# Kernel optimization log

Measured on AMD Instinct MI355X. Metric: run time of the kernel, lower is better.

The kernel has to match this reference:

```python
import jax, jax.numpy as jnp
import numpy as np
import math

B, S, HID, NH = 2, 2048, 1024, 16
HD = HID // NH


def setup_inputs() -> dict:
    key = jax.random.key(0)
    ks = jax.random.split(key, 6)
    scale = 0.02
    return {
        "hidden_states": jax.random.normal(ks[0], (B, S, HID), dtype=jnp.float32),
        "attention_mask": jnp.ones((B, S), dtype=jnp.float32),
        "Wq": jax.random.normal(ks[1], (HID, HID), dtype=jnp.float32) * scale,
        "bq": jnp.zeros((HID,), dtype=jnp.float32),
        "Wk": jax.random.normal(ks[2], (HID, HID), dtype=jnp.float32) * scale,
        "bk": jnp.zeros((HID,), dtype=jnp.float32),
        "Wv": jax.random.normal(ks[3], (HID, HID), dtype=jnp.float32) * scale,
        "bv": jnp.zeros((HID,), dtype=jnp.float32),
        "Wo": jax.random.normal(ks[4], (HID, HID), dtype=jnp.float32) * scale,
        "bo": jnp.zeros((HID,), dtype=jnp.float32),
        "beta": jnp.zeros((1,), dtype=jnp.float32),
        "gamma": jnp.ones((1,), dtype=jnp.float32),
    }


def reference(hidden_states, attention_mask, Wq, bq, Wk, bk, Wv, bv, Wo, bo, beta, gamma):
    b, s, h = hidden_states.shape

    def proj(W, bias):
        # torch Linear: x @ W.T + b ; then split heads -> [B, NH, S, HD]
        y = jnp.einsum('bsh,oh->bso', hidden_states, W) + bias
        return y.reshape(b, s, NH, HD).transpose(0, 2, 1, 3)

    q = proj(Wq, bq)
    k = proj(Wk, bk)
    v = proj(Wv, bv)

    scores = jnp.einsum('bnsd,bntd->bnst', q, k) / math.sqrt(HD)  # [B,NH,S,S]
    # extended mask: [B,1,1,S]; additive -1e4 on masked positions
    scores = scores + (1.0 - attention_mask)[:, None, None, :] * (-10000.0)

    # ConsMax: exp(scores - beta - rowmax) / gamma (no sum normalization)
    shifted = scores - beta
    shifted = shifted - jnp.max(shifted, axis=-1, keepdims=True)
    probs = jnp.exp(shifted) / gamma  # dropout p=0 -> identity

    ctx = jnp.einsum('bnst,bntd->bnsd', probs, v)  # [B,NH,S,HD]
    ctx = ctx.transpose(0, 2, 1, 3).reshape(b, s, h)
    return jnp.einsum('bsh,oh->bso', ctx, Wo) + bo
```

## Files before the change

kernel.cpp:

```cpp
#include <hip/hip_runtime.h>
#include <hip/hip_bf16.h>


typedef unsigned short u16;
typedef __attribute__((ext_vector_type(8))) short short8;
typedef __attribute__((ext_vector_type(4))) float floatx4;
typedef __attribute__((ext_vector_type(16))) float floatx16;

constexpr int B_  = 2;
constexpr int S_  = 2048;
constexpr int HID = 1024;
constexpr int NH  = 16;
constexpr int HD  = 64;

constexpr float LOG2E   = 1.4426950408889634f;
constexpr float QSCALE  = 0.125f * LOG2E;
constexpr float MSCALE  = -10000.0f * LOG2E;

#if __has_builtin(__builtin_amdgcn_exp2f)
#define EXP2(x) __builtin_amdgcn_exp2f(x)
#else
#define EXP2(x) exp2f(x)
#endif

__device__ __forceinline__ u16 f2us(float f) {
    union { float f; unsigned int i; } x;
    x.f = f;
    unsigned int r = x.i + 0x7FFFu + ((x.i >> 16) & 1u);
    return (u16)(r >> 16);
}
__device__ __forceinline__ unsigned pk2(float a, float b) {
    __hip_bfloat162 h = __float22bfloat162_rn(make_float2(a, b));
    unsigned u; __builtin_memcpy(&u, &h, 4); return u;
}
__device__ __forceinline__ void async_lds16(const u16* g, u16* l) {
    __builtin_amdgcn_global_load_lds(
        (const __attribute__((address_space(1))) unsigned int*)g,
        (__attribute__((address_space(3))) unsigned int*)l, 16, 0, 0);
}

__global__ __launch_bounds__(256)
void cvt_all(const float* __restrict__ hs, const float* __restrict__ Wq,
             const float* __restrict__ Wk, const float* __restrict__ Wv,
             const float* __restrict__ Wo,
             u16* __restrict__ hs_bf, u16* __restrict__ Wcat,
             u16* __restrict__ Wo_bf)
{
    const int bid = blockIdx.x;
    const float* src;
    u16* dst;
    size_t base;
    if (bid < 4096) {
        src = hs; dst = hs_bf; base = (size_t)bid * 1024;
    } else if (bid < 7168) {
        const int s = (bid - 4096) >> 10;
        src = (s == 0) ? Wq : (s == 1) ? Wk : Wv;
        dst = Wcat + (size_t)s * 1048576;
        base = (size_t)((bid - 4096) & 1023) * 1024;
    } else {
        src = Wo; dst = Wo_bf; base = (size_t)(bid - 7168) * 1024;
    }
    const size_t i = base + threadIdx.x * 4;
    float4 t = *(const float4*)(src + i);
    uint2 o = { pk2(t.x, t.y), pk2(t.z, t.w) };
    *(uint2*)(dst + i) = o;
}

__global__ __launch_bounds__(256)
void qkv_gemm(const u16* __restrict__ hs_bf, const u16* __restrict__ Wcat,
              const float* __restrict__ bq, const float* __restrict__ bk,
              const float* __restrict__ bv,
              u16* __restrict__ Qo, u16* __restrict__ Ko, u16* __restrict__ VT)
{
    __shared__ u16 Alds[8192];
    __shared__ u16 Blds[8192];

    const int tid = threadIdx.x;
    const int id  = blockIdx.x;
    const int xcd = id & 7, jb = id >> 3;
    const int m0  = (xcd * 4 + (jb & 3)) * 128;
    const int n0g = (jb >> 2) * 128;
    const int p   = n0g >> 10;
    const int n0  = n0g & 1023;
    const u16*   Wb = Wcat + (size_t)p * 1048576;
    const float* bi = (p == 0) ? bq : (p == 1) ? bk : bv;
    const float  osc = (p == 0) ? QSCALE : 1.0f;

    const int w = tid >> 6, l = tid & 63;
    const int quad = l >> 4, l16 = l & 15;
    const int wy = w >> 1, wx = w & 1;

    floatx4 acc[4][4];
    #pragma unroll
    for (int i = 0; i < 4; ++i)
        #pragma unroll
        for (int j = 0; j < 4; ++j) acc[i][j] = (floatx4){0.f, 0.f, 0.f, 0.f};

    for (int k0 = 0; k0 < HID; k0 += 64) {
        __syncthreads();
        #pragma unroll
        for (int c = 0; c < 2; ++c) {
            const int s = w * 2 + c;
            #pragma unroll
            for (int t = 0; t < 2; ++t) {
                async_lds16(hs_bf + (size_t)(m0 + s * 16 + l16) * HID + k0 + t * 32 + quad * 8,
                            &Alds[s * 1024 + t * 512]);
                async_lds16(Wb + (size_t)(n0 + s * 16 + l16) * HID + k0 + t * 32 + quad * 8,
                            &Blds[s * 1024 + t * 512]);
            }
        }
        __syncthreads();

        #pragma unroll
        for (int t = 0; t < 2; ++t) {
            short8 afr[4], bfr[4];
            #pragma unroll
            for (int i = 0; i < 4; ++i)
                afr[i] = *(const short8*)&Alds[(wy*4 + i) * 1024 + t * 512 + l * 8];
            #pragma unroll
            for (int j = 0; j < 4; ++j)
                bfr[j] = *(const short8*)&Blds[(wx*4 + j) * 1024 + t * 512 + l * 8];
            #pragma unroll
            for (int i = 0; i < 4; ++i)
                #pragma unroll
                for (int j = 0; j < 4; ++j)
                    acc[i][j] = __builtin_amdgcn_mfma_f32_16x16x32_bf16(afr[i], bfr[j], acc[i][j], 0, 0, 0);
        }
    }

    #pragma unroll
    for (int i = 0; i < 4; ++i)
        #pragma unroll
        for (int j = 0; j < 4; ++j) {
            const int nn   = n0 + wx * 64 + j * 16 + l16;
            const int head = nn >> 6, dd = nn & 63;
            const float bb_ = bi[nn];
            const int mmb = m0 + wy * 64 + i * 16 + quad * 4;
            const int b = mmb >> 11, ss = mmb & (S_ - 1);
            if (p == 2) {
                uint2 st = { pk2(acc[i][j][0] + bb_, acc[i][j][1] + bb_),
                             pk2(acc[i][j][2] + bb_, acc[i][j][3] + bb_) };
                *(uint2*)(VT + (((size_t)(b * NH + head)) * HD + dd) * S_ + ss) = st;
            } else {
                u16* Out = (p == 0) ? Qo : Ko;
                #pragma unroll
                for (int rg = 0; rg < 4; ++rg)
                    Out[(((size_t)b * NH + head) * S_ + ss + rg) * HD + dd] =
                        f2us((acc[i][j][rg] + bb_) * osc);
            }
        }
}

__global__ __launch_bounds__(256, 2)
void attn12(const u16* __restrict__ Qg, const u16* __restrict__ Kg,
            const u16* __restrict__ VTg, const float* __restrict__ mask,
            const float* __restrict__ gamma, u16* __restrict__ ctx)
{
    __shared__ u16 Kb[3][4096];
    __shared__ u16 Vb[3][4096];
    __shared__ u16 Pq[8192];
    __shared__ float Mb[2048];

    const int tid = threadIdx.x;
    const int w = tid >> 6, l = tid & 63;
    const int l32 = l & 31, hh = l >> 5;
    const int swz = (l32 & 7) << 3;
    const int id  = blockIdx.x;
    const int xcd = id & 7, jb = id >> 3;
    const int bh  = xcd * 4 + (jb >> 4);
    const int qb  = jb & 15;
    const int b0  = bh >> 4, h = bh & (NH - 1);

    const u16* Qb    = Qg  + (size_t)bh * S_ * HD;
    const u16* Kbg   = Kg  + (size_t)bh * S_ * HD;
    const u16* Vbg   = VTg + (size_t)bh * HD * S_;
    const float* mG  = mask + (size_t)b0 * S_;

    const int qrow = qb * 128 + w * 32 + l32;

    short8 qB[4];
    #pragma unroll
    for (int dc = 0; dc < 4; ++dc)
        qB[dc] = *(const short8*)(Qb + (size_t)qrow * HD + dc * 16 + hh * 8);

    {
        float4 ma = *(const float4*)(mG + tid * 8);
        float4 mb2 = *(const float4*)(mG + tid * 8 + 4);
        float* d = &Mb[tid * 8];
        d[0] = fmaf(ma.x, -MSCALE, MSCALE);
        d[1] = fmaf(ma.y, -MSCALE, MSCALE);
        d[2] = fmaf(ma.z, -MSCALE, MSCALE);
        d[3] = fmaf(ma.w, -MSCALE, MSCALE);
        d[4] = fmaf(mb2.x, -MSCALE, MSCALE);
        d[5] = fmaf(mb2.y, -MSCALE, MSCALE);
        d[6] = fmaf(mb2.z, -MSCALE, MSCALE);
        d[7] = fmaf(mb2.w, -MSCALE, MSCALE);
    }

    floatx16 oacc[2];
    #pragma unroll
    for (int db = 0; db < 2; ++db)
        #pragma unroll
        for (int i = 0; i < 16; ++i) oacc[db][i] = 0.f;
    float m_run = -1e30f;

    u16* Pw = Pq + w * 2048;

    auto stage = [&](int kt, int bf) {
        #pragma unroll
        for (int c = 0; c < 2; ++c) {
            const int r = w * 2 + c;
            const int kb = r >> 2, dc = r & 3;
            async_lds16(Kbg + (size_t)(kt * 64 + kb * 32 + l32) * HD + dc * 16 + hh * 8,
                        &Kb[bf][r * 512]);
            const int db = r >> 2, kg = r & 3;
            async_lds16(Vbg + (size_t)(db * 32 + l32) * S_ + kt * 64 + kg * 16 + hh * 8,
                        &Vb[bf][r * 512]);
        }
    };

    __syncthreads();
    constexpr int NT = S_ / 64;
    stage(0, 0);
    stage(1, 1);

    for (int kt = 0; kt < NT; ++kt) {
        const int cur = kt % 3;
        if (kt < NT - 1) asm volatile("s_waitcnt vmcnt(4)" ::: "memory");
        else             asm volatile("s_waitcnt vmcnt(0)" ::: "memory");
        __builtin_amdgcn_s_barrier();
        if (kt + 2 < NT) stage(kt + 2, (kt + 2) % 3);

        #pragma unroll
        for (int kb = 0; kb < 2; ++kb) {
            const float* mrow = &Mb[kt * 64 + kb * 32 + 4 * hh];
            floatx16 acc;
            #pragma unroll
            for (int g = 0; g < 4; ++g) {
                float4 mv = *(const float4*)(mrow + g * 8);
                acc[4*g]   = mv.x;
                acc[4*g+1] = mv.y;
                acc[4*g+2] = mv.z;
                acc[4*g+3] = mv.w;
            }
            #pragma unroll
            for (int dc = 0; dc < 4; ++dc) {
                short8 kf = *(const short8*)&Kb[cur][(kb * 4 + dc) * 512 + l * 8];
                acc = __builtin_amdgcn_mfma_f32_32x32x16_bf16(kf, qB[dc], acc, 0, 0, 0);
            }
            float mr = m_run;
            #pragma unroll
            for (int i = 0; i < 16; ++i) mr = fmaxf(mr, acc[i]);
            m_run = mr;
            #pragma unroll
            for (int g = 0; g < 4; ++g) {
                uint2 pw = { pk2(EXP2(acc[4*g]),   EXP2(acc[4*g+1])),
                             pk2(EXP2(acc[4*g+2]), EXP2(acc[4*g+3])) };
                const int koff = kb * 32 + 8 * g + 4 * hh;
                *(uint2*)&Pw[l32 * 64 + (koff ^ swz)] = pw;
            }
        }

        #pragma unroll
        for (int kg = 0; kg < 4; ++kg) {
            short8 pf = *(const short8*)&Pw[l32 * 64 + ((kg * 16 + hh * 8) ^ swz)];
            #pragma unroll
            for (int db = 0; db < 2; ++db) {
                short8 vf = *(const short8*)&Vb[cur][(db * 4 + kg) * 512 + l * 8];
                oacc[db] = __builtin_amdgcn_mfma_f32_32x32x16_bf16(vf, pf, oacc[db], 0, 0, 0);
            }
        }
    }

    const float mx = fmaxf(m_run, __shfl_xor(m_run, 32, 64));
    const float si = EXP2(-mx) * (1.0f / gamma[0]);
    u16* crow = ctx + (size_t)(b0 * S_ + qrow) * HID + h * HD;
    #pragma unroll
    for (int db = 0; db < 2; ++db)
        #pragma unroll
        for (int g = 0; g < 4; ++g) {
            uint2 st = { pk2(oacc[db][g * 4 + 0] * si, oacc[db][g * 4 + 1] * si),
                         pk2(oacc[db][g * 4 + 2] * si, oacc[db][g * 4 + 3] * si) };
            *(uint2*)(crow + db * 32 + g * 8 + hh * 4) = st;
        }
}

__global__ __launch_bounds__(256)
void out_gemm(const u16* __restrict__ ctx, const u16* __restrict__ Wo_bf,
              const float* __restrict__ bo, float* __restrict__ out)
{
    __shared__ u16 Alds[8192];
    __shared__ u16 Blds[4096];

    const int tid = threadIdx.x;
    const int id  = blockIdx.x;
    const int xcd = id & 7, jb = id >> 3;
    const int m0  = (xcd * 4 + (jb & 3)) * 128;
    const int n0  = (jb >> 2) * 64;

    const int w = tid >> 6, l = tid & 63;
    const int quad = l >> 4, l16 = l & 15;

    floatx4 acc[2][4];
    #pragma unroll
    for (int i = 0; i < 2; ++i)
        #pragma unroll
        for (int j = 0; j < 4; ++j) acc[i][j] = (floatx4){0.f, 0.f, 0.f, 0.f};

    for (int k0 = 0; k0 < HID; k0 += 64) {
        __syncthreads();
        #pragma unroll
        for (int c = 0; c < 2; ++c) {
            const int s = w * 2 + c;
            #pragma unroll
            for (int t = 0; t < 2; ++t)
                async_lds16(ctx + (size_t)(m0 + s * 16 + l16) * HID + k0 + t * 32 + quad * 8,
                            &Alds[s * 1024 + t * 512]);
        }
        #pragma unroll
        for (int t = 0; t < 2; ++t)
            async_lds16(Wo_bf + (size_t)(n0 + w * 16 + l16) * HID + k0 + t * 32 + quad * 8,
                        &Blds[w * 1024 + t * 512]);
        __syncthreads();

        #pragma unroll
        for (int t = 0; t < 2; ++t) {
            short8 afr[2], bfr[4];
            #pragma unroll
            for (int i = 0; i < 2; ++i)
                afr[i] = *(const short8*)&Alds[(w*2 + i) * 1024 + t * 512 + l * 8];
            #pragma unroll
            for (int j = 0; j < 4; ++j)
                bfr[j] = *(const short8*)&Blds[j * 1024 + t * 512 + l * 8];
            #pragma unroll
            for (int i = 0; i < 2; ++i)
                #pragma unroll
                for (int j = 0; j < 4; ++j)
                    acc[i][j] = __builtin_amdgcn_mfma_f32_16x16x32_bf16(afr[i], bfr[j], acc[i][j], 0, 0, 0);
        }
    }

    #pragma unroll
    for (int i = 0; i < 2; ++i)
        #pragma unroll
        for (int j = 0; j < 4; ++j) {
            const int nn = n0 + j * 16 + l16;
            const float bb_ = bo[nn];
            #pragma unroll
            for (int rg = 0; rg < 4; ++rg) {
                const int mm = m0 + w * 32 + i * 16 + quad * 4 + rg;
                out[(size_t)mm * HID + nn] = acc[i][j][rg] + bb_;
            }
        }
}

extern "C" void kernel_launch(void* const* d_in, const int* in_sizes, int n_in,
                              void* d_out, int out_size, void* d_ws, size_t ws_size,
                              hipStream_t stream)
{
    const float* hs    = (const float*)d_in[0];
    const float* mask  = (const float*)d_in[1];
    const float* Wq    = (const float*)d_in[2];
    const float* bq    = (const float*)d_in[3];
    const float* Wk    = (const float*)d_in[4];
    const float* bk    = (const float*)d_in[5];
    const float* Wv    = (const float*)d_in[6];
    const float* bv    = (const float*)d_in[7];
    const float* Wo    = (const float*)d_in[8];
    const float* bo    = (const float*)d_in[9];
    const float* gamma = (const float*)d_in[11];
    float* out = (float*)d_out;

    const size_t tsz = (size_t)B_ * NH * S_ * HD;
    u16* q     = (u16*)d_ws;
    u16* vT    = q + tsz;
    u16* Wcat  = vT + tsz;
    u16* Wo_bf = Wcat + 3u * 1048576u;
    u16* ctx   = Wo_bf + 1048576u;
    u16* hs_bf = (u16*)d_out;
    u16* kbuf  = hs_bf + tsz;

    cvt_all<<<dim3(8192), 256, 0, stream>>>(hs, Wq, Wk, Wv, Wo, hs_bf, Wcat, Wo_bf);
    qkv_gemm<<<dim3(768), 256, 0, stream>>>(hs_bf, Wcat, bq, bk, bv, q, kbuf, vT);
    attn12<<<dim3(512), 256, 0, stream>>>(q, kbuf, vT, mask, gamma, ctx);
    out_gemm<<<dim3(512), 256, 0, stream>>>(ctx, Wo_bf, bo, out);
}
```

Before: 245.6 us.

## Triple-buffer LDS with async prefetch in QKV and output GEMMs

Both projection GEMMs move from a single LDS buffer with two full barriers per 64-wide K step to a three-stage ring of 32-wide K slices. Loads for slice ks+2 are issued while slice ks is being computed, gated by explicit vmcnt waits and one barrier per step. The aim is to overlap global-to-LDS traffic with MFMA work instead of stalling on each load. In exchange it uses more LDS, runs twice as many loop iterations with fewer MFMAs each, and depends on hand-counted vmcnt values being correct.

```diff
diff --git a/kernel.cpp b/kernel.cpp
--- a/kernel.cpp
+++ b/kernel.cpp
@@ -72,8 +72,8 @@
               const float* __restrict__ bv,
               u16* __restrict__ Qo, u16* __restrict__ Ko, u16* __restrict__ VT)
 {
-    __shared__ u16 Alds[8192];
-    __shared__ u16 Blds[8192];
+    __shared__ u16 Alds[3][4096];
+    __shared__ u16 Blds[3][4096];
 
     const int tid = threadIdx.x;
     const int id  = blockIdx.x;
@@ -96,36 +96,41 @@
         #pragma unroll
         for (int j = 0; j < 4; ++j) acc[i][j] = (floatx4){0.f, 0.f, 0.f, 0.f};
 
-    for (int k0 = 0; k0 < HID; k0 += 64) {
-        __syncthreads();
+    auto stage = [&](int ks, int bf) {
+        const int k0 = ks * 32;
         #pragma unroll
         for (int c = 0; c < 2; ++c) {
             const int s = w * 2 + c;
-            #pragma unroll
-            for (int t = 0; t < 2; ++t) {
-                async_lds16(hs_bf + (size_t)(m0 + s * 16 + l16) * HID + k0 + t * 32 + quad * 8,
-                            &Alds[s * 1024 + t * 512]);
-                async_lds16(Wb + (size_t)(n0 + s * 16 + l16) * HID + k0 + t * 32 + quad * 8,
-                            &Blds[s * 1024 + t * 512]);
-            }
-        }
-        __syncthreads();
-
-        #pragma unroll
-        for (int t = 0; t < 2; ++t) {
-            short8 afr[4], bfr[4];
-            #pragma unroll
-            for (int i = 0; i < 4; ++i)
-                afr[i] = *(const short8*)&Alds[(wy*4 + i) * 1024 + t * 512 + l * 8];
+            async_lds16(hs_bf + (size_t)(m0 + s * 16 + l16) * HID + k0 + quad * 8,
+                        &Alds[bf][s * 512]);
+            async_lds16(Wb + (size_t)(n0 + s * 16 + l16) * HID + k0 + quad * 8,
+                        &Blds[bf][s * 512]);
+        }
+    };
+
+    constexpr int NS = HID / 32;
+    stage(0, 0);
+    stage(1, 1);
+
+    for (int ks = 0; ks < NS; ++ks) {
+        const int cur = ks % 3;
+        if (ks < NS - 1) asm volatile("s_waitcnt vmcnt(4)" ::: "memory");
+        else             asm volatile("s_waitcnt vmcnt(0)" ::: "memory");
+        __builtin_amdgcn_s_barrier();
+        if (ks + 2 < NS) stage(ks + 2, (ks + 2) % 3);
+
+        short8 afr[4], bfr[4];
+        #pragma unroll
+        for (int i = 0; i < 4; ++i)
+            afr[i] = *(const short8*)&Alds[cur][(wy * 4 + i) * 512 + l * 8];
+        #pragma unroll
+        for (int j = 0; j < 4; ++j)
+            bfr[j] = *(const short8*)&Blds[cur][(wx * 4 + j) * 512 + l * 8];
+        #pragma unroll
+        for (int i = 0; i < 4; ++i)
             #pragma unroll
             for (int j = 0; j < 4; ++j)
-                bfr[j] = *(const short8*)&Blds[(wx*4 + j) * 1024 + t * 512 + l * 8];
-            #pragma unroll
-            for (int i = 0; i < 4; ++i)
-                #pragma unroll
-                for (int j = 0; j < 4; ++j)
-                    acc[i][j] = __builtin_amdgcn_mfma_f32_16x16x32_bf16(afr[i], bfr[j], acc[i][j], 0, 0, 0);
-        }
+                acc[i][j] = __builtin_amdgcn_mfma_f32_16x16x32_bf16(afr[i], bfr[j], acc[i][j], 0, 0, 0);
     }
 
     #pragma unroll
@@ -289,8 +294,8 @@
 void out_gemm(const u16* __restrict__ ctx, const u16* __restrict__ Wo_bf,
               const float* __restrict__ bo, float* __restrict__ out)
 {
-    __shared__ u16 Alds[8192];
-    __shared__ u16 Blds[4096];
+    __shared__ u16 Alds[3][4096];
+    __shared__ u16 Blds[3][2048];
 
     const int tid = threadIdx.x;
     const int id  = blockIdx.x;
@@ -307,37 +312,41 @@
         #pragma unroll
         for (int j = 0; j < 4; ++j) acc[i][j] = (floatx4){0.f, 0.f, 0.f, 0.f};
 
-    for (int k0 = 0; k0 < HID; k0 += 64) {
-        __syncthreads();
+    auto stage = [&](int ks, int bf) {
+        const int k0 = ks * 32;
         #pragma unroll
         for (int c = 0; c < 2; ++c) {
             const int s = w * 2 + c;
-            #pragma unroll
-            for (int t = 0; t < 2; ++t)
-                async_lds16(ctx + (size_t)(m0 + s * 16 + l16) * HID + k0 + t * 32 + quad * 8,
-                            &Alds[s * 1024 + t * 512]);
-        }
-        #pragma unroll
-        for (int t = 0; t < 2; ++t)
-            async_lds16(Wo_bf + (size_t)(n0 + w * 16 + l16) * HID + k0 + t * 32 + quad * 8,
-                        &Blds[w * 1024 + t * 512]);
-        __syncthreads();
-
-        #pragma unroll
-        for (int t = 0; t < 2; ++t) {
-            short8 afr[2], bfr[4];
-            #pragma unroll
-            for (int i = 0; i < 2; ++i)
-                afr[i] = *(const short8*)&Alds[(w*2 + i) * 1024 + t * 512 + l * 8];
+            async_lds16(ctx + (size_t)(m0 + s * 16 + l16) * HID + k0 + quad * 8,
+                        &Alds[bf][s * 512]);
+        }
+        async_lds16(Wo_bf + (size_t)(n0 + w * 16 + l16) * HID + k0 + quad * 8,
+                    &Blds[bf][w * 512]);
+    };
+
+    constexpr int NS = HID / 32;
+    stage(0, 0);
+    stage(1, 1);
+
+    for (int ks = 0; ks < NS; ++ks) {
+        const int cur = ks % 3;
+        if (ks < NS - 1) asm volatile("s_waitcnt vmcnt(3)" ::: "memory");
+        else             asm volatile("s_waitcnt vmcnt(0)" ::: "memory");
+        __builtin_amdgcn_s_barrier();
+        if (ks + 2 < NS) stage(ks + 2, (ks + 2) % 3);
+
+        short8 afr[2], bfr[4];
+        #pragma unroll
+        for (int i = 0; i < 2; ++i)
+            afr[i] = *(const short8*)&Alds[cur][(w * 2 + i) * 512 + l * 8];
+        #pragma unroll
+        for (int j = 0; j < 4; ++j)
+            bfr[j] = *(const short8*)&Blds[cur][j * 512 + l * 8];
+        #pragma unroll
+        for (int i = 0; i < 2; ++i)
             #pragma unroll
             for (int j = 0; j < 4; ++j)
-                bfr[j] = *(const short8*)&Blds[j * 1024 + t * 512 + l * 8];
-            #pragma unroll
-            for (int i = 0; i < 2; ++i)
-                #pragma unroll
-                for (int j = 0; j < 4; ++j)
-                    acc[i][j] = __builtin_amdgcn_mfma_f32_16x16x32_bf16(afr[i], bfr[j], acc[i][j], 0, 0, 0);
-        }
+                acc[i][j] = __builtin_amdgcn_mfma_f32_16x16x32_bf16(afr[i], bfr[j], acc[i][j], 0, 0, 0);
     }
 
     #pragma unroll
```

After: 238.9 us. -2.7%, faster.
